# Kernel tuning notes

Measured on AMD Instinct MI355X. Metric: run time of the kernel, lower is better.

Reference implementation:

```python
import jax, jax.numpy as jnp
import numpy as np

H = 128
N0 = 32768
N1 = 32768
N = N0 + N1
E = 524288
R = 4
L = 2
BS = 1024
PER = N // BS


def setup_inputs() -> dict:
    key = jax.random.key(0)
    ks = jax.random.split(key, 20)
    s = 1.0 / np.sqrt(H)
    x0 = jax.random.normal(ks[0], (N0, H), jnp.float32)
    x1 = jax.random.normal(ks[1], (N1, H), jnp.float32)
    W0 = jax.random.normal(ks[2], (H, H), jnp.float32) * s
    W1 = jax.random.normal(ks[3], (H, H), jnp.float32) * s
    conv_root = jax.random.normal(ks[4], (L, H, H), jnp.float32) * s
    conv_rel = jax.random.normal(ks[5], (L, R, H, H), jnp.float32) * s
    attW = jax.random.normal(ks[6], (L, R * R, H, H), jnp.float32) * s
    att_q = jax.random.normal(ks[7], (L, R * R, H), jnp.float32) * s
    att_k = jax.random.normal(ks[8], (L, R * R, H), jnp.float32) * s
    fc_W = jax.random.normal(ks[9], (H, H), jnp.float32) * s
    src = jax.random.randint(ks[10], (E,), 0, N)
    dst = jax.random.randint(ks[11], (E,), 0, N)
    edge_index = jnp.stack([src, dst], 0)
    edge_type = jax.random.randint(ks[12], (E,), 0, R)
    # mask: ones, but zero the first node of ~half the samples (mirrors torch.rand(batch)<0.5)
    drop = jax.random.uniform(ks[13], (BS,)) < 0.5
    row_mask = jnp.where(drop[:, None, None] & (jnp.arange(PER)[None, :, None] == 0), 0.0, 1.0)
    mask = jnp.broadcast_to(row_mask, (BS, PER, H)).reshape(N, H).astype(jnp.float32)
    return {
        "x0": x0, "x1": x1, "W0": W0, "b0": jnp.zeros((H,), jnp.float32),
        "W1": W1, "b1": jnp.zeros((H,), jnp.float32), "mask": mask,
        "conv_root": conv_root, "conv_rel": conv_rel, "conv_b": jnp.zeros((L, H), jnp.float32),
        "attW": attW, "att_q": att_q, "att_k": att_k, "att_b": jnp.zeros((L, H), jnp.float32),
        "bn_g": jnp.ones((L, H), jnp.float32), "bn_b": jnp.zeros((L, H), jnp.float32),
        "fc_W": fc_W, "fc_b": jnp.zeros((H,), jnp.float32),
        "edge_index": edge_index, "edge_type": edge_type, "batch_size": BS,
    }


def reference(x0, x1, W0, b0, W1, b1, mask, conv_root, conv_rel, conv_b,
              attW, att_q, att_k, att_b, bn_g, bn_b, fc_W, fc_b,
              edge_index, edge_type, batch_size):
    n = x0.shape[0] + x1.shape[0]
    r = conv_rel.shape[1]
    # per-node-type linear transforms, then to_homogeneous concat
    x_in = jnp.concatenate([x0 @ W0 + b0, x1 @ W1 + b1], axis=0)  # [N,H]
    src, dst = edge_index[0], edge_index[1]
    seg = dst * r + edge_type  # (target node, relation) segments
    x = x_in
    for l in range(conv_root.shape[0]):
        xm = x * mask
        # ---- RGCNConv: per-relation transform, mean aggregation per relation, root + bias
        xr = jnp.einsum('nh,rho->rno', xm, conv_rel[l])  # [R,N,H]
        m = xr[edge_type, src]  # [E,H]
        s = jax.ops.segment_sum(m, seg, num_segments=n * r)
        cnt = jax.ops.segment_sum(jnp.ones((seg.shape[0],), m.dtype), seg, num_segments=n * r)
        agg = (s / jnp.maximum(cnt, 1.0)[:, None]).reshape(n, r, -1).sum(1)
        x_conv = agg + xm @ conv_root[l] + conv_b[l]
        # ---- RGATConv (heads=1, within-relation softmax, additive self-attention)
        xa = jnp.einsum('nh,rho->rno', xm, attW[l, :r])  # only real edge types used
        sq = jnp.einsum('rnh,rh->rn', xa, att_q[l, :r])
        sk = jnp.einsum('rnh,rh->rn', xa, att_k[l, :r])
        logit = jax.nn.leaky_relu(sq[edge_type, dst] + sk[edge_type, src], 0.2)  # [E]
        mx = jax.ops.segment_max(logit, seg, num_segments=n * r)
        mx = jnp.where(jnp.isfinite(mx), mx, 0.0)
        ex = jnp.exp(logit - mx[seg])
        den = jax.ops.segment_sum(ex, seg, num_segments=n * r)
        alpha = ex / jnp.maximum(den[seg], 1e-16)
        x_att = jax.ops.segment_sum(alpha[:, None] * xa[edge_type, src], dst, num_segments=n) + att_b[l]
        # ---- BatchNorm (training stats) + leaky_relu(0.01)
        h = x_conv + x_att
        mu = h.mean(0)
        var = h.var(0)
        h = (h - mu) / jnp.sqrt(var + 1e-5) * bn_g[l] + bn_b[l]
        x = jax.nn.leaky_relu(h, 0.01)
    out = (x + x_in) @ fc_W + fc_b
    out = out.reshape(batch_size, -1, out.shape[-1])
    return out[:, 0], out[:, 1:, :]
```

## Files before the change

kernel.cpp:

```cpp
#include <hip/hip_runtime.h>

#define Hd 128
#define NTOT 65536
#define RREL 4
#define NRSEG (NTOT*RREL)
#define NEDGE 524288

typedef unsigned short u16;
typedef unsigned int u32;
typedef short bf16x8 __attribute__((ext_vector_type(8)));
typedef float f32x4 __attribute__((ext_vector_type(4)));

__device__ __forceinline__ u16 f2bf(float f) {
  u32 u = __float_as_uint(f);
  return (u16)((u + 0x7fffu + ((u >> 16) & 1u)) >> 16);
}
__device__ __forceinline__ u32 pack2(float lo, float hi) {
  return ((u32)f2bf(hi) << 16) | f2bf(lo);
}

__device__ __forceinline__ int swzb(int row, int o) {
  return (row*256 + o) ^ ((row & 15) << 4);
}

__device__ __forceinline__ void stage_tile(const u16* __restrict__ g, int ld,
                                           u16* lds, int wave, int lane) {
#pragma unroll
  for (int t = 0; t < 2; ++t) {
    int i = wave*2 + t;
    int row = i*16 + (lane >> 2);
    int col16 = (lane & 3) ^ ((lane >> 3) & 3);
    const u16* src = g + (size_t)row*ld + col16*8;
    __builtin_amdgcn_global_load_lds((const __attribute__((address_space(1))) void*)src,
                                     (__attribute__((address_space(3))) void*)(lds + i*512),
                                     16, 0, 0);
  }
}

template<int CMODE>
__global__ __launch_bounds__(256) void mgemm(const u16* __restrict__ A, int lda,
                                             const u16* __restrict__ Bt, int ldb,
                                             const float* __restrict__ bias,
                                             const float* __restrict__ bias2,
                                             float* __restrict__ C, int kTot)
{
  __shared__ u16 As[4096], Bs[4096];
  const int tid = threadIdx.x, wave = tid >> 6, lane = tid & 63;
  const int wm = wave >> 1, wn = wave & 1;
  int bx = blockIdx.x;
  if (CMODE == 3) {
    if (bx >= (int)gridDim.x/2) {
      bx -= gridDim.x/2;
      A += (size_t)32768*lda; Bt += 128*128; bias = bias2; C += (size_t)32768*Hd;
    }
  }
  const int brow = bx * 128;
  const u16* Ab = A + (size_t)brow*lda;
  f32x4 acc[4][4];
#pragma unroll
  for (int i = 0; i < 4; ++i)
#pragma unroll
    for (int j = 0; j < 4; ++j) acc[i][j] = (f32x4){0.f, 0.f, 0.f, 0.f};

  const int ks = (lane >> 4) * 16;
  const int rl = lane & 15;
  for (int k0 = 0; k0 < kTot; k0 += 32) {
    stage_tile(Ab + k0, lda, As, wave, lane);
    stage_tile(Bt + k0, ldb, Bs, wave, lane);
    __syncthreads();
    bf16x8 af[4], bv[4];
    const char* Ac = (const char*)As;
    const char* Bc = (const char*)Bs;
#pragma unroll
    for (int i = 0; i < 4; ++i) {
      int r = wm*64 + i*16 + rl;
      int by = (r*64 + ks) ^ (((r >> 1) & 3) << 4);
      af[i] = *(const bf16x8*)(Ac + by);
    }
#pragma unroll
    for (int j = 0; j < 4; ++j) {
      int r = wn*64 + j*16 + rl;
      int by = (r*64 + ks) ^ (((r >> 1) & 3) << 4);
      bv[j] = *(const bf16x8*)(Bc + by);
    }
#pragma unroll
    for (int i = 0; i < 4; ++i)
#pragma unroll
      for (int j = 0; j < 4; ++j)
        acc[i][j] = __builtin_amdgcn_mfma_f32_16x16x32_bf16(af[i], bv[j], acc[i][j], 0, 0, 0);
    __syncthreads();
  }
  const int cl = lane & 15;
  const int rq = (lane >> 4) * 4;
#pragma unroll
  for (int i = 0; i < 4; ++i) {
#pragma unroll
    for (int q = 0; q < 4; ++q) {
      int row = brow + wm*64 + i*16 + rq + q;
      size_t ob;
      if (CMODE == 2) {
        int b = row >> 6, p = row & 63;
        ob = (p == 0) ? (size_t)b*Hd
                      : (size_t)(1024*Hd) + ((size_t)(b*63 + (p-1)))*Hd;
      } else {
        ob = (size_t)row * Hd;
      }
#pragma unroll
      for (int j = 0; j < 4; ++j) {
        int col = wn*64 + j*16 + cl;
        float v = acc[i][j][q];
        if (bias) v += bias[col];
        C[ob + col] = v;
      }
    }
  }
}

__device__ __forceinline__ void stageB(const u16* __restrict__ gbase, int ld,
                                       u16* lds, int wave, int lane) {
#pragma unroll
  for (int t = 0; t < 4; ++t) {
    int ti = wave*4 + t;
    int row = ti*4 + (lane >> 4);
    int lchunk = (lane & 15) ^ (row & 15);
    const u16* src = gbase + (size_t)row*ld + lchunk*8;
    __builtin_amdgcn_global_load_lds((const __attribute__((address_space(1))) void*)src,
                                     (__attribute__((address_space(3))) void*)(lds + ti*512),
                                     16, 0, 0);
  }
}
__device__ __forceinline__ void stageY64(const u16* __restrict__ gbase, int ld,
                                         u16* lds, int wave, int lane) {
#pragma unroll
  for (int t = 0; t < 2; ++t) {
    int ti = wave*2 + t;
    int row = ti*4 + (lane >> 4);
    int lchunk = (lane & 15) ^ (row & 15);
    const u16* src = gbase + (size_t)row*ld + lchunk*8;
    __builtin_amdgcn_global_load_lds((const __attribute__((address_space(1))) void*)src,
                                     (__attribute__((address_space(3))) void*)(lds + ti*512),
                                     16, 0, 0);
  }
}

__device__ __forceinline__ void mfma64(const u16* Yt, const u16* Bt, f32x4 (&acc)[2][2],
                                       int wm, int wn, int lane) {
  const int rl = lane & 15;
  const int ko = (lane >> 4) * 16;
  const char* Yc_ = (const char*)Yt;
  const char* Bc_ = (const char*)Bt;
#pragma unroll
  for (int ks = 0; ks < 4; ++ks) {
    int o = ks*64 + ko;
    bf16x8 af[2], bv[2];
#pragma unroll
    for (int i = 0; i < 2; ++i)
      af[i] = *(const bf16x8*)(Yc_ + swzb(wm*32 + i*16 + rl, o));
#pragma unroll
    for (int j = 0; j < 2; ++j)
      bv[j] = *(const bf16x8*)(Bc_ + swzb(wn*32 + j*16 + rl, o));
#pragma unroll
    for (int i = 0; i < 2; ++i)
#pragma unroll
      for (int j = 0; j < 2; ++j)
        acc[i][j] = __builtin_amdgcn_mfma_f32_16x16x32_bf16(af[i], bv[j], acc[i][j], 0, 0, 0);
  }
}

__global__ __launch_bounds__(512, 2) void fused_gemm(
    const u16* __restrict__ xmb, const int* __restrict__ src_sorted,
    const float* __restrict__ exs, const int* __restrict__ offsets,
    const u16* __restrict__ Btg, float* __restrict__ hbuf, float* __restrict__ bns)
{
  __shared__ u16 Yt[8192];
  __shared__ u16 Bw[16384];
  const int tid = threadIdx.x, wave = tid >> 6, lane = tid & 63;
  const int wm = wave >> 2, wn = wave & 3;
  const int brow = blockIdx.x * 64;
  f32x4 acc[2][2];
#pragma unroll
  for (int i = 0; i < 2; ++i)
#pragma unroll
    for (int j = 0; j < 2; ++j) acc[i][j] = (f32x4){0.f, 0.f, 0.f, 0.f};

  u32 axp[8];

  for (int r = 0; r < RREL; ++r) {
    __syncthreads();
    stageB(Btg + r*128, 1152, Bw, wave, lane);
#pragma unroll
    for (int g = 0; g < 4; ++g) {
      int ln0 = wave*8 + g*2;
      int e0[2], ct[2];
#pragma unroll
      for (int m = 0; m < 2; ++m) {
        int seg = (brow + ln0 + m)*RREL + r;
        e0[m] = offsets[seg];
        ct[m] = offsets[seg+1] - e0[m];
      }
      int   si[2][4];
      float ew[2][4];
#pragma unroll
      for (int m = 0; m < 2; ++m)
#pragma unroll
        for (int k = 0; k < 4; ++k) {
          si[m][k] = src_sorted[e0[m] + k];
          ew[m][k] = exs[e0[m] + k];
        }
      u32 uu[2][4];
#pragma unroll
      for (int m = 0; m < 2; ++m)
#pragma unroll
        for (int k = 0; k < 4; ++k) {
          int sx = (k < ct[m]) ? si[m][k] : 0;
          uu[m][k] = *(const u32*)(xmb + (size_t)sx*Hd + lane*2);
        }
      float cx[2], cy[2], ax[2], ay[2];
#pragma unroll
      for (int m = 0; m < 2; ++m) { cx[m] = cy[m] = ax[m] = ay[m] = 0.f; }
#pragma unroll
      for (int m = 0; m < 2; ++m) {
#pragma unroll
        for (int k = 0; k < 4; ++k) {
          float pr = (k < ct[m]) ? 1.f : 0.f;
          float al = pr * ew[m][k];
          float vx = __uint_as_float(uu[m][k] << 16);
          float vy = __uint_as_float(uu[m][k] & 0xffff0000u);
          cx[m] = fmaf(pr, vx, cx[m]);
          cy[m] = fmaf(pr, vy, cy[m]);
          ax[m] = fmaf(al, vx, ax[m]);
          ay[m] = fmaf(al, vy, ay[m]);
        }
        for (int e = e0[m] + 4; e < e0[m] + ct[m]; ++e) {
          int s = src_sorted[e];
          float al = exs[e];
          u32 u = *(const u32*)(xmb + (size_t)s*Hd + lane*2);
          float vx = __uint_as_float(u << 16);
          float vy = __uint_as_float(u & 0xffff0000u);
          cx[m] += vx; cy[m] += vy;
          ax[m] = fmaf(al, vx, ax[m]);
          ay[m] = fmaf(al, vy, ay[m]);
        }
      }
#pragma unroll
      for (int m = 0; m < 2; ++m) {
        int ln = ln0 + m;
        float ic = 1.f / (float)max(ct[m], 1);
        *(u32*)((char*)Yt + swzb(ln, lane*4)) = pack2(cx[m]*ic, cy[m]*ic);
        axp[g*2+m] = pack2(ax[m], ay[m]);
      }
    }
    __syncthreads();
    mfma64(Yt, Bw, acc, wm, wn, lane);
    __syncthreads();
    stageB(Btg + (4+r)*128, 1152, Bw, wave, lane);
#pragma unroll
    for (int g = 0; g < 4; ++g)
#pragma unroll
      for (int m = 0; m < 2; ++m) {
        int ln = wave*8 + g*2 + m;
        *(u32*)((char*)Yt + swzb(ln, lane*4)) = axp[g*2+m];
      }
    __syncthreads();
    mfma64(Yt, Bw, acc, wm, wn, lane);
  }
  __syncthreads();
  stageY64(xmb + (size_t)brow*Hd, Hd, Yt, wave, lane);
  stageB(Btg + 8*128, 1152, Bw, wave, lane);
  __syncthreads();
  mfma64(Yt, Bw, acc, wm, wn, lane);

  const int cl = lane & 15, rq = (lane >> 4) * 4;
#pragma unroll
  for (int j = 0; j < 2; ++j) {
    float s = 0.f, s2 = 0.f;
#pragma unroll
    for (int i = 0; i < 2; ++i) {
#pragma unroll
      for (int q = 0; q < 4; ++q) {
        float v = acc[i][j][q];
        int row = brow + wm*32 + i*16 + rq + q;
        hbuf[(size_t)row*Hd + wn*32 + j*16 + cl] = v;
        s += v; s2 = fmaf(v, v, s2);
      }
    }
    s  += __shfl_xor(s, 16);  s  += __shfl_xor(s, 32);
    s2 += __shfl_xor(s2, 16); s2 += __shfl_xor(s2, 32);
    if (lane < 16) {
      int col = wn*32 + j*16 + cl;
      unsafeAtomicAdd(&bns[col], s);
      unsafeAtomicAdd(&bns[128 + col], s2);
    }
  }
}

__global__ void wtrans(const float* __restrict__ B, u16* __restrict__ Bt,
                       int K, int ldb, int koff) {
  int idx = blockIdx.x*256 + threadIdx.x;
  if (idx >= K*128) return;
  int k = idx >> 7, o = idx & 127;
  Bt[(size_t)o*ldb + koff + k] = f2bf(B[idx]);
}

__global__ void fill_i32(int* p, int v, int n) {
  int i = blockIdx.x*blockDim.x + threadIdx.x;
  if (i < n) p[i] = v;
}
__global__ void rowmask_k(const float* __restrict__ mask, float* __restrict__ rm) {
  int n = blockIdx.x*blockDim.x + threadIdx.x;
  if (n < NTOT) rm[n] = mask[(size_t)n*Hd];
}
__global__ void edge_count(const int* __restrict__ dst, const int* __restrict__ et, int* __restrict__ cnt) {
  int e = blockIdx.x*blockDim.x + threadIdx.x;
  if (e < NEDGE) atomicAdd(&cnt[dst[e]*RREL + et[e]], 1);
}
__global__ void cvt_bf16_2(const float* __restrict__ s0, const float* __restrict__ s1,
                           u16* __restrict__ dst) {
  int i = blockIdx.x*256 + threadIdx.x;
  const int half = 32768*Hd/4;
  const float* s = (i < half) ? s0 : s1;
  int ii = (i < half) ? i : i - half;
  float4 v = *reinterpret_cast<const float4*>(s + (size_t)ii*4);
  *reinterpret_cast<uint2*>(dst + (size_t)i*4) = make_uint2(pack2(v.x, v.y), pack2(v.z, v.w));
}
__global__ void mkxmb(const float* __restrict__ x, const float* __restrict__ rm,
                      u16* __restrict__ xmb) {
  int i = blockIdx.x*256 + threadIdx.x;
  float s = rm[i >> 5];
  float4 v = *reinterpret_cast<const float4*>(x + (size_t)i*4);
  *reinterpret_cast<uint2*>(xmb + (size_t)i*4) =
      make_uint2(pack2(v.x*s, v.y*s), pack2(v.z*s, v.w*s));
}

__global__ void scan1_k(const int* __restrict__ cnt, int* __restrict__ partial, int* __restrict__ bsum) {
  __shared__ int sh[256];
  int t = threadIdx.x;
  int i = blockIdx.x*256 + t;
  int v = cnt[i];
  sh[t] = v; __syncthreads();
  for (int off = 1; off < 256; off <<= 1) {
    int u = (t >= off) ? sh[t-off] : 0;
    __syncthreads();
    sh[t] += u;
    __syncthreads();
  }
  partial[i] = sh[t] - v;
  if (t == 255) bsum[blockIdx.x] = sh[255];
}
__global__ void scan2_k(int* __restrict__ bsum) {
  __shared__ int sh[256];
  int t = threadIdx.x;
  int v0 = bsum[t*4+0], v1 = bsum[t*4+1], v2 = bsum[t*4+2], v3 = bsum[t*4+3];
  int tot = v0+v1+v2+v3;
  sh[t] = tot; __syncthreads();
  for (int off = 1; off < 256; off <<= 1) {
    int u = (t >= off) ? sh[t-off] : 0;
    __syncthreads();
    sh[t] += u;
    __syncthreads();
  }
  int base = sh[t] - tot;
  bsum[t*4+0] = base;
  bsum[t*4+1] = base + v0;
  bsum[t*4+2] = base + v0+v1;
  bsum[t*4+3] = base + v0+v1+v2;
}
__global__ void scan3_k(const int* __restrict__ partial, const int* __restrict__ bsum, int* __restrict__ offsets) {
  int i = blockIdx.x*256 + threadIdx.x;
  offsets[i] = partial[i] + bsum[i >> 8];
  if (i == 0) offsets[NRSEG] = NEDGE;
}
__global__ void csr_fill(const int* __restrict__ src, const int* __restrict__ dst,
                         const int* __restrict__ et, const int* __restrict__ offsets,
                         int* __restrict__ fillctr, int* __restrict__ src_sorted) {
  int e = blockIdx.x*blockDim.x + threadIdx.x;
  if (e >= NEDGE) return;
  int seg = dst[e]*RREL + et[e];
  int pos = offsets[seg] + atomicAdd(&fillctr[seg], 1);
  src_sorted[pos] = src[e];
}

__global__ void qkvec_k(const float* __restrict__ attW, const float* __restrict__ att_q,
                        const float* __restrict__ att_k,
                        float* __restrict__ qvec, float* __restrict__ kvec,
                        float* __restrict__ bns) {
  int t = threadIdx.x;
  if (t < 256) bns[t] = 0.f;
  int r = t >> 7, h = t & 127;
  const float* wrow = attW + ((size_t)r*Hd + h)*Hd;
  const float* qv = att_q + (size_t)r*Hd;
  const float* kv = att_k + (size_t)r*Hd;
  float sq_ = 0.f, sk_ = 0.f;
  for (int o = 0; o < Hd; ++o) { float w = wrow[o]; sq_ = fmaf(w, qv[o], sq_); sk_ = fmaf(w, kv[o], sk_); }
  qvec[r*Hd + h] = sq_;
  kvec[r*Hd + h] = sk_;
}

__global__ void sqk_k(const u16* __restrict__ xmb, const float* __restrict__ qvec,
                      const float* __restrict__ kvec, float* __restrict__ sq, float* __restrict__ sk) {
  int w = blockIdx.x*4 + (threadIdx.x >> 6);
  if (w >= NTOT) return;
  int lane = threadIdx.x & 63;
  u32 u = *reinterpret_cast<const u32*>(xmb + (size_t)w*Hd + lane*2);
  float vx = __uint_as_float(u << 16);
  float vy = __uint_as_float(u & 0xffff0000u);
  float pq[RREL], pk[RREL];
#pragma unroll
  for (int r = 0; r < RREL; ++r) {
    float2 q = *reinterpret_cast<const float2*>(qvec + r*Hd + lane*2);
    float2 k = *reinterpret_cast<const float2*>(kvec + r*Hd + lane*2);
    pq[r] = vx*q.x + vy*q.y;
    pk[r] = vx*k.x + vy*k.y;
  }
#pragma unroll
  for (int off = 32; off > 0; off >>= 1) {
#pragma unroll
    for (int r = 0; r < RREL; ++r) {
      pq[r] += __shfl_xor(pq[r], off);
      pk[r] += __shfl_xor(pk[r], off);
    }
  }
  if (lane == 0) {
#pragma unroll
    for (int r = 0; r < RREL; ++r) {
      sq[(size_t)r*NTOT + w] = pq[r];
      sk[(size_t)r*NTOT + w] = pk[r];
    }
  }
}

__global__ void seg_alpha(const int* __restrict__ src_sorted, const int* __restrict__ offsets,
                          const float* __restrict__ sq, const float* __restrict__ sk,
                          float* __restrict__ exs) {
  int seg = blockIdx.x*256 + threadIdx.x;
  if (seg >= NRSEG) return;
  int e0 = offsets[seg], e1 = offsets[seg+1];
  if (e0 == e1) return;
  int nd = seg >> 2, r = seg & 3;
  float sqv = sq[(size_t)r*NTOT + nd];
  float sum = 0.f;
  for (int e = e0; e < e1; ++e) {
    float lg = sqv + sk[(size_t)r*NTOT + src_sorted[e]];
    lg = lg >= 0.f ? lg : 0.2f*lg;
    float ex = __expf(lg);
    exs[e] = ex;
    sum += ex;
  }
  float inv = 1.f / fmaxf(sum, 1e-16f);
  for (int e = e0; e < e1; ++e) exs[e] *= inv;
}

__global__ void bn_final(const float* __restrict__ bns, const float* __restrict__ g,
                         const float* __restrict__ b, float* __restrict__ scale,
                         float* __restrict__ shift) {
  int c = threadIdx.x;
  float mu = bns[c] * (1.f/NTOT);
  float var = bns[128 + c] * (1.f/NTOT) - mu*mu;
  float sc = g[c] / sqrtf(var + 1e-5f);
  scale[c] = sc;
  shift[c] = b[c] - mu*sc;
}

template<int LAST>
__global__ void bn_apply(const float* __restrict__ h, const float* __restrict__ scale,
                         const float* __restrict__ shift, const float* __restrict__ rm,
                         const float* __restrict__ x_in, u16* __restrict__ xmb) {
  int i = blockIdx.x*256 + threadIdx.x;
  size_t i4 = (size_t)i*4;
  int c = (int)(i4 & 127);
  float4 v = *reinterpret_cast<const float4*>(h + i4);
  float4 sc = *reinterpret_cast<const float4*>(scale + c);
  float4 sh = *reinterpret_cast<const float4*>(shift + c);
  v.x = fmaf(v.x, sc.x, sh.x); v.y = fmaf(v.y, sc.y, sh.y);
  v.z = fmaf(v.z, sc.z, sh.z); v.w = fmaf(v.w, sc.w, sh.w);
  v.x = v.x >= 0.f ? v.x : 0.01f*v.x;
  v.y = v.y >= 0.f ? v.y : 0.01f*v.y;
  v.z = v.z >= 0.f ? v.z : 0.01f*v.z;
  v.w = v.w >= 0.f ? v.w : 0.01f*v.w;
  float4 xb;
  if (LAST) {
    float4 rsd = *reinterpret_cast<const float4*>(x_in + i4);
    xb.x = v.x + rsd.x; xb.y = v.y + rsd.y; xb.z = v.z + rsd.z; xb.w = v.w + rsd.w;
  } else {
    float s = rm[i >> 5];
    xb.x = v.x*s; xb.y = v.y*s; xb.z = v.z*s; xb.w = v.w*s;
  }
  *reinterpret_cast<uint2*>(xmb + i4) = make_uint2(pack2(xb.x, xb.y), pack2(xb.z, xb.w));
}

extern "C" void kernel_launch(void* const* d_in, const int* in_sizes, int n_in,
                              void* d_out, int out_size, void* d_ws, size_t ws_size,
                              hipStream_t stream) {
  const float* x0       = (const float*)d_in[0];
  const float* x1       = (const float*)d_in[1];
  const float* W0       = (const float*)d_in[2];
  const float* b0       = (const float*)d_in[3];
  const float* W1       = (const float*)d_in[4];
  const float* b1       = (const float*)d_in[5];
  const float* mask     = (const float*)d_in[6];
  const float* conv_root= (const float*)d_in[7];
  const float* conv_rel = (const float*)d_in[8];
  const float* attW     = (const float*)d_in[10];
  const float* att_q    = (const float*)d_in[11];
  const float* att_k    = (const float*)d_in[12];
  const float* bn_g     = (const float*)d_in[14];
  const float* bn_b     = (const float*)d_in[15];
  const float* fc_W     = (const float*)d_in[16];
  const float* fc_b     = (const float*)d_in[17];
  const int* edge_index = (const int*)d_in[18];
  const int* edge_type  = (const int*)d_in[19];
  const int* src = edge_index;
  const int* dst = edge_index + NEDGE;
  (void)in_sizes; (void)n_in; (void)out_size; (void)ws_size;

  char* ws = (char*)d_ws;
  size_t off = 0;
  auto alloc = [&](size_t bytes) { void* p = ws + off; off = (off + bytes + 255) & ~(size_t)255; return p; };
  float* x_in  = (float*)alloc((size_t)NTOT*Hd*4);
  float* hbuf  = (float*)alloc((size_t)NTOT*Hd*4);
  u16*   xmb   = (u16*)  alloc((size_t)NTOT*Hd*2);
  float* sq    = (float*)alloc((size_t)RREL*NTOT*4);
  float* sk    = (float*)alloc((size_t)RREL*NTOT*4);
  float* exs   = (float*)alloc((size_t)(NEDGE+16)*4);
  float* rm    = (float*)alloc((size_t)NTOT*4);
  int* cnt        = (int*)alloc((size_t)NRSEG*4);
  int* fillctr    = (int*)alloc((size_t)NRSEG*4);
  int* partial    = (int*)alloc((size_t)NRSEG*4);
  int* offsets    = (int*)alloc((size_t)(NRSEG+4)*4);
  int* bsum       = (int*)alloc(4096);
  int* src_sorted = (int*)alloc((size_t)(NEDGE+16)*4);
  float* qvec   = (float*)alloc(512*4);
  float* kvec   = (float*)alloc(512*4);
  float* bns    = (float*)alloc(1024);
  float* bnscale= (float*)alloc(512);
  float* bnshift= (float*)alloc(512);
  u16* Btw  = (u16*)alloc((size_t)2*128*128*2);
  u16* Btg0 = (u16*)alloc((size_t)128*1152*2);
  u16* Btg1 = (u16*)alloc((size_t)128*1152*2);
  u16* BtgL[2] = {Btg0, Btg1};

  rowmask_k<<<NTOT/256, 256, 0, stream>>>(mask, rm);
  fill_i32<<<NRSEG/256, 256, 0, stream>>>(cnt, 0, NRSEG);
  edge_count<<<NEDGE/256, 256, 0, stream>>>(dst, edge_type, cnt);
  scan1_k<<<NRSEG/256, 256, 0, stream>>>(cnt, partial, bsum);
  scan2_k<<<1, 256, 0, stream>>>(bsum);
  scan3_k<<<NRSEG/256, 256, 0, stream>>>(partial, bsum, offsets);
  fill_i32<<<NRSEG/256, 256, 0, stream>>>(fillctr, 0, NRSEG);
  csr_fill<<<NEDGE/256, 256, 0, stream>>>(src, dst, edge_type, offsets, fillctr, src_sorted);

  for (int l = 0; l < 2; ++l) {
    wtrans<<<(512*128)/256, 256, 0, stream>>>(conv_rel + (size_t)l*RREL*Hd*Hd, BtgL[l], 512, 1152, 0);
    wtrans<<<(512*128)/256, 256, 0, stream>>>(attW + (size_t)l*16*Hd*Hd, BtgL[l], 512, 1152, 512);
    wtrans<<<(128*128)/256, 256, 0, stream>>>(conv_root + (size_t)l*Hd*Hd, BtgL[l], 128, 1152, 1024);
  }

  cvt_bf16_2<<<(NTOT*Hd/4)/256, 256, 0, stream>>>(x0, x1, xmb);
  wtrans<<<(128*128)/256, 256, 0, stream>>>(W0, Btw, 128, 128, 0);
  wtrans<<<(128*128)/256, 256, 0, stream>>>(W1, Btw + 128*128, 128, 128, 0);
  mgemm<3><<<512, 256, 0, stream>>>(xmb, Hd, Btw, 128, b0, b1, x_in, 128);
  mkxmb<<<(NTOT*Hd/4)/256, 256, 0, stream>>>(x_in, rm, xmb);

  for (int l = 0; l < 2; ++l) {
    const float* attW_l = attW + (size_t)l*16*Hd*Hd;
    qkvec_k<<<1, 512, 0, stream>>>(attW_l, att_q + (size_t)l*16*Hd, att_k + (size_t)l*16*Hd,
                                   qvec, kvec, bns);
    sqk_k<<<NTOT/4, 256, 0, stream>>>(xmb, qvec, kvec, sq, sk);
    seg_alpha<<<NRSEG/256, 256, 0, stream>>>(src_sorted, offsets, sq, sk, exs);
    fused_gemm<<<NTOT/64, 512, 0, stream>>>(xmb, src_sorted, exs, offsets,
                                            BtgL[l], hbuf, bns);
    bn_final<<<1, 128, 0, stream>>>(bns, bn_g + (size_t)l*Hd, bn_b + (size_t)l*Hd, bnscale, bnshift);
    if (l == 0)
      bn_apply<0><<<(NTOT*Hd/4)/256, 256, 0, stream>>>(hbuf, bnscale, bnshift, rm, x_in, xmb);
    else
      bn_apply<1><<<(NTOT*Hd/4)/256, 256, 0, stream>>>(hbuf, bnscale, bnshift, rm, x_in, xmb);
  }

  wtrans<<<(128*128)/256, 256, 0, stream>>>(fc_W, Btw, 128, 128, 0);
  mgemm<2><<<512, 256, 0, stream>>>(xmb, Hd, Btw, 128, fc_b, nullptr, (float*)d_out, 128);
}
```

Measured before the change: 482.3 us.

## Restructure RGCN layer kernels with relation-major CSR and LDS atomic aggregation

Switches the segment layout to relation-major and packs source and destination into one 32-bit meta word per edge. The fused GEMM now handles 32 rows per block and spreads edge aggregation across waves using float atomics in LDS, instead of per-node loops in registers. Separately, weight transposes are merged into one launch, q/k vectors for both layers are precomputed, and the BN apply is fused with the attention-score computation. This cuts launch count, tail imbalance on uneven degrees and a full pass over xmb, at the cost of LDS atomic contention and a 16-bit packing limit on node ids.

```diff
diff --git a/kernel.cpp b/kernel.cpp
--- a/kernel.cpp
+++ b/kernel.cpp
@@ -129,21 +129,17 @@
                                      16, 0, 0);
   }
 }
-__device__ __forceinline__ void stageY64(const u16* __restrict__ gbase, int ld,
+__device__ __forceinline__ void stageY32(const u16* __restrict__ gbase, int ld,
                                          u16* lds, int wave, int lane) {
-#pragma unroll
-  for (int t = 0; t < 2; ++t) {
-    int ti = wave*2 + t;
-    int row = ti*4 + (lane >> 4);
-    int lchunk = (lane & 15) ^ (row & 15);
-    const u16* src = gbase + (size_t)row*ld + lchunk*8;
-    __builtin_amdgcn_global_load_lds((const __attribute__((address_space(1))) void*)src,
-                                     (__attribute__((address_space(3))) void*)(lds + ti*512),
-                                     16, 0, 0);
-  }
-}
-
-__device__ __forceinline__ void mfma64(const u16* Yt, const u16* Bt, f32x4 (&acc)[2][2],
+  int row = wave*4 + (lane >> 4);
+  int lchunk = (lane & 15) ^ (row & 15);
+  const u16* src = gbase + (size_t)row*ld + lchunk*8;
+  __builtin_amdgcn_global_load_lds((const __attribute__((address_space(1))) void*)src,
+                                   (__attribute__((address_space(3))) void*)(lds + wave*512),
+                                   16, 0, 0);
+}
+
+__device__ __forceinline__ void mfma32(const u16* Yt, const u16* Bt, f32x4 (&acc)[2],
                                        int wm, int wn, int lane) {
   const int rl = lane & 15;
   const int ko = (lane >> 4) * 16;
@@ -152,137 +148,116 @@
 #pragma unroll
   for (int ks = 0; ks < 4; ++ks) {
     int o = ks*64 + ko;
-    bf16x8 af[2], bv[2];
-#pragma unroll
-    for (int i = 0; i < 2; ++i)
-      af[i] = *(const bf16x8*)(Yc_ + swzb(wm*32 + i*16 + rl, o));
-#pragma unroll
-    for (int j = 0; j < 2; ++j)
-      bv[j] = *(const bf16x8*)(Bc_ + swzb(wn*32 + j*16 + rl, o));
-#pragma unroll
-    for (int i = 0; i < 2; ++i)
-#pragma unroll
-      for (int j = 0; j < 2; ++j)
-        acc[i][j] = __builtin_amdgcn_mfma_f32_16x16x32_bf16(af[i], bv[j], acc[i][j], 0, 0, 0);
+    bf16x8 af = *(const bf16x8*)(Yc_ + swzb(wm*16 + rl, o));
+    bf16x8 b0 = *(const bf16x8*)(Bc_ + swzb(wn*32 + rl, o));
+    bf16x8 b1 = *(const bf16x8*)(Bc_ + swzb(wn*32 + 16 + rl, o));
+    acc[0] = __builtin_amdgcn_mfma_f32_16x16x32_bf16(af, b0, acc[0], 0, 0, 0);
+    acc[1] = __builtin_amdgcn_mfma_f32_16x16x32_bf16(af, b1, acc[1], 0, 0, 0);
   }
 }
 
 __global__ __launch_bounds__(512, 2) void fused_gemm(
-    const u16* __restrict__ xmb, const int* __restrict__ src_sorted,
+    const u16* __restrict__ xmb, const u32* __restrict__ meta,
     const float* __restrict__ exs, const int* __restrict__ offsets,
     const u16* __restrict__ Btg, float* __restrict__ hbuf, float* __restrict__ bns)
 {
-  __shared__ u16 Yt[8192];
-  __shared__ u16 Bw[16384];
+  __shared__ float Ycf[4096];
+  __shared__ float Yaf[4096];
+  __shared__ u16  Ybf[4096];
+  __shared__ u16  Bw[16384];
   const int tid = threadIdx.x, wave = tid >> 6, lane = tid & 63;
   const int wm = wave >> 2, wn = wave & 3;
-  const int brow = blockIdx.x * 64;
-  f32x4 acc[2][2];
-#pragma unroll
-  for (int i = 0; i < 2; ++i)
-#pragma unroll
-    for (int j = 0; j < 2; ++j) acc[i][j] = (f32x4){0.f, 0.f, 0.f, 0.f};
-
-  u32 axp[8];
+  const int brow = blockIdx.x * 32;
+  f32x4 acc[2];
+  acc[0] = (f32x4){0.f,0.f,0.f,0.f};
+  acc[1] = (f32x4){0.f,0.f,0.f,0.f};
+
+  {
+    float4 z = {0.f,0.f,0.f,0.f};
+#pragma unroll
+    for (int t = 0; t < 2; ++t) {
+      *(float4*)(Ycf + tid*4 + t*2048) = z;
+      *(float4*)(Yaf + tid*4 + t*2048) = z;
+    }
+  }
+  const int prow = tid >> 4;
+  const int pc2  = (tid & 15) * 8;
+  const int pX   = (prow & 7) << 2;
 
   for (int r = 0; r < RREL; ++r) {
+    const int segBase = (r << 16) + brow;
     __syncthreads();
     stageB(Btg + r*128, 1152, Bw, wave, lane);
-#pragma unroll
-    for (int g = 0; g < 4; ++g) {
-      int ln0 = wave*8 + g*2;
-      int e0[2], ct[2];
-#pragma unroll
-      for (int m = 0; m < 2; ++m) {
-        int seg = (brow + ln0 + m)*RREL + r;
-        e0[m] = offsets[seg];
-        ct[m] = offsets[seg+1] - e0[m];
+    float ic;
+    {
+      int a = offsets[segBase + prow], b = offsets[segBase + prow + 1];
+      ic = 1.f / (float)max(b - a, 1);
+    }
+    {
+      int eB = offsets[segBase], eE = offsets[segBase + 32];
+      for (int e = eB + wave; e < eE; e += 8) {
+        u32 md = meta[e];
+        float al = exs[e];
+        int s  = md & 0xffff;
+        int ln = (int)(md >> 16) - brow;
+        u32 u = *(const u32*)(xmb + ((size_t)s << 7) + lane*2);
+        float vx = __uint_as_float(u << 16);
+        float vy = __uint_as_float(u & 0xffff0000u);
+        int fi = ((ln << 7) + lane*2) ^ ((ln & 7) << 2);
+        unsafeAtomicAdd(&Ycf[fi],     vx);
+        unsafeAtomicAdd(&Ycf[fi + 1], vy);
+        unsafeAtomicAdd(&Yaf[fi],     al*vx);
+        unsafeAtomicAdd(&Yaf[fi + 1], al*vy);
       }
-      int   si[2][4];
-      float ew[2][4];
-#pragma unroll
-      for (int m = 0; m < 2; ++m)
-#pragma unroll
-        for (int k = 0; k < 4; ++k) {
-          si[m][k] = src_sorted[e0[m] + k];
-          ew[m][k] = exs[e0[m] + k];
-        }
-      u32 uu[2][4];
-#pragma unroll
-      for (int m = 0; m < 2; ++m)
-#pragma unroll
-        for (int k = 0; k < 4; ++k) {
-          int sx = (k < ct[m]) ? si[m][k] : 0;
-          uu[m][k] = *(const u32*)(xmb + (size_t)sx*Hd + lane*2);
-        }
-      float cx[2], cy[2], ax[2], ay[2];
-#pragma unroll
-      for (int m = 0; m < 2; ++m) { cx[m] = cy[m] = ax[m] = ay[m] = 0.f; }
-#pragma unroll
-      for (int m = 0; m < 2; ++m) {
-#pragma unroll
-        for (int k = 0; k < 4; ++k) {
-          float pr = (k < ct[m]) ? 1.f : 0.f;
-          float al = pr * ew[m][k];
-          float vx = __uint_as_float(uu[m][k] << 16);
-          float vy = __uint_as_float(uu[m][k] & 0xffff0000u);
-          cx[m] = fmaf(pr, vx, cx[m]);
-          cy[m] = fmaf(pr, vy, cy[m]);
-          ax[m] = fmaf(al, vx, ax[m]);
-          ay[m] = fmaf(al, vy, ay[m]);
-        }
-        for (int e = e0[m] + 4; e < e0[m] + ct[m]; ++e) {
-          int s = src_sorted[e];
-          float al = exs[e];
-          u32 u = *(const u32*)(xmb + (size_t)s*Hd + lane*2);
-          float vx = __uint_as_float(u << 16);
-          float vy = __uint_as_float(u & 0xffff0000u);
-          cx[m] += vx; cy[m] += vy;
-          ax[m] = fmaf(al, vx, ax[m]);
-          ay[m] = fmaf(al, vy, ay[m]);
-        }
-      }
-#pragma unroll
-      for (int m = 0; m < 2; ++m) {
-        int ln = ln0 + m;
-        float ic = 1.f / (float)max(ct[m], 1);
-        *(u32*)((char*)Yt + swzb(ln, lane*4)) = pack2(cx[m]*ic, cy[m]*ic);
-        axp[g*2+m] = pack2(ax[m], ay[m]);
-      }
-    }
-    __syncthreads();
-    mfma64(Yt, Bw, acc, wm, wn, lane);
+    }
+    __syncthreads();
+    {
+      int base = prow*128 + pc2;
+      int i0 = base ^ pX, i1 = (base + 4) ^ pX;
+      float4 v0 = *(float4*)(Ycf + i0);
+      float4 v1 = *(float4*)(Ycf + i1);
+      *(float4*)(Ycf + i0) = (float4){0.f,0.f,0.f,0.f};
+      *(float4*)(Ycf + i1) = (float4){0.f,0.f,0.f,0.f};
+      uint4 o;
+      o.x = pack2(v0.x*ic, v0.y*ic); o.y = pack2(v0.z*ic, v0.w*ic);
+      o.z = pack2(v1.x*ic, v1.y*ic); o.w = pack2(v1.z*ic, v1.w*ic);
+      *(uint4*)((char*)Ybf + swzb(prow, pc2*2)) = o;
+    }
+    __syncthreads();
+    mfma32(Ybf, Bw, acc, wm, wn, lane);
     __syncthreads();
     stageB(Btg + (4+r)*128, 1152, Bw, wave, lane);
-#pragma unroll
-    for (int g = 0; g < 4; ++g)
-#pragma unroll
-      for (int m = 0; m < 2; ++m) {
-        int ln = wave*8 + g*2 + m;
-        *(u32*)((char*)Yt + swzb(ln, lane*4)) = axp[g*2+m];
-      }
-    __syncthreads();
-    mfma64(Yt, Bw, acc, wm, wn, lane);
+    {
+      int base = prow*128 + pc2;
+      int i0 = base ^ pX, i1 = (base + 4) ^ pX;
+      float4 v0 = *(float4*)(Yaf + i0);
+      float4 v1 = *(float4*)(Yaf + i1);
+      *(float4*)(Yaf + i0) = (float4){0.f,0.f,0.f,0.f};
+      *(float4*)(Yaf + i1) = (float4){0.f,0.f,0.f,0.f};
+      uint4 o;
+      o.x = pack2(v0.x, v0.y); o.y = pack2(v0.z, v0.w);
+      o.z = pack2(v1.x, v1.y); o.w = pack2(v1.z, v1.w);
+      *(uint4*)((char*)Ybf + swzb(prow, pc2*2)) = o;
+    }
+    __syncthreads();
+    mfma32(Ybf, Bw, acc, wm, wn, lane);
   }
   __syncthreads();
-  stageY64(xmb + (size_t)brow*Hd, Hd, Yt, wave, lane);
+  stageY32(xmb + ((size_t)brow << 7), Hd, Ybf, wave, lane);
   stageB(Btg + 8*128, 1152, Bw, wave, lane);
   __syncthreads();
-  mfma64(Yt, Bw, acc, wm, wn, lane);
+  mfma32(Ybf, Bw, acc, wm, wn, lane);
 
   const int cl = lane & 15, rq = (lane >> 4) * 4;
 #pragma unroll
   for (int j = 0; j < 2; ++j) {
     float s = 0.f, s2 = 0.f;
 #pragma unroll
-    for (int i = 0; i < 2; ++i) {
-#pragma unroll
-      for (int q = 0; q < 4; ++q) {
-        float v = acc[i][j][q];
-        int row = brow + wm*32 + i*16 + rq + q;
-        hbuf[(size_t)row*Hd + wn*32 + j*16 + cl] = v;
-        s += v; s2 = fmaf(v, v, s2);
-      }
+    for (int q = 0; q < 4; ++q) {
+      float v = acc[j][q];
+      int row = brow + wm*16 + rq + q;
+      hbuf[(size_t)row*Hd + wn*32 + j*16 + cl] = v;
+      s += v; s2 = fmaf(v, v, s2);
     }
     s  += __shfl_xor(s, 16);  s  += __shfl_xor(s, 32);
     s2 += __shfl_xor(s2, 16); s2 += __shfl_xor(s2, 32);
@@ -294,12 +269,27 @@
   }
 }
 
-__global__ void wtrans(const float* __restrict__ B, u16* __restrict__ Bt,
-                       int K, int ldb, int koff) {
+__global__ void wtrans_all(const float* __restrict__ conv_rel, const float* __restrict__ attW,
+                           const float* __restrict__ conv_root, const float* __restrict__ W0,
+                           const float* __restrict__ W1, const float* __restrict__ fcW,
+                           u16* __restrict__ Btg0, u16* __restrict__ Btg1, u16* __restrict__ Btw) {
   int idx = blockIdx.x*256 + threadIdx.x;
-  if (idx >= K*128) return;
-  int k = idx >> 7, o = idx & 127;
-  Bt[(size_t)o*ldb + koff + k] = f2bf(B[idx]);
+  if (idx < 294912) {
+    int l = idx / 147456;
+    int rem = idx - l*147456;
+    u16* Btg = l ? Btg1 : Btg0;
+    float v; int o, kk;
+    if (rem < 65536)       { o = rem & 127; kk = rem >> 7;               v = conv_rel[(size_t)l*65536 + rem]; }
+    else if (rem < 131072) { int r2 = rem - 65536; o = r2 & 127; kk = 512 + (r2 >> 7); v = attW[(size_t)l*262144 + r2]; }
+    else                   { int r3 = rem - 131072; o = r3 & 127; kk = 1024 + (r3 >> 7); v = conv_root[(size_t)l*16384 + r3]; }
+    Btg[(size_t)o*1152 + kk] = f2bf(v);
+  } else {
+    int rem = idx - 294912;
+    int w = rem >> 14, r3 = rem & 16383;
+    int k = r3 >> 7, o = r3 & 127;
+    const float* sp = (w == 0) ? W0 : (w == 1 ? W1 : fcW);
+    Btw[w*16384 + o*128 + k] = f2bf(sp[r3]);
+  }
 }
 
 __global__ void fill_i32(int* p, int v, int n) {
@@ -312,7 +302,7 @@
 }
 __global__ void edge_count(const int* __restrict__ dst, const int* __restrict__ et, int* __restrict__ cnt) {
   int e = blockIdx.x*blockDim.x + threadIdx.x;
-  if (e < NEDGE) atomicAdd(&cnt[dst[e]*RREL + et[e]], 1);
+  if (e < NEDGE) atomicAdd(&cnt[(et[e] << 16) + dst[e]], 1);
 }
 __global__ void cvt_bf16_2(const float* __restrict__ s0, const float* __restrict__ s1,
                            u16* __restrict__ dst) {
@@ -323,14 +313,6 @@
   float4 v = *reinterpret_cast<const float4*>(s + (size_t)ii*4);
   *reinterpret_cast<uint2*>(dst + (size_t)i*4) = make_uint2(pack2(v.x, v.y), pack2(v.z, v.w));
 }
-__global__ void mkxmb(const float* __restrict__ x, const float* __restrict__ rm,
-                      u16* __restrict__ xmb) {
-  int i = blockIdx.x*256 + threadIdx.x;
-  float s = rm[i >> 5];
-  float4 v = *reinterpret_cast<const float4*>(x + (size_t)i*4);
-  *reinterpret_cast<uint2*>(xmb + (size_t)i*4) =
-      make_uint2(pack2(v.x*s, v.y*s), pack2(v.z*s, v.w*s));
-}
 
 __global__ void scan1_k(const int* __restrict__ cnt, int* __restrict__ partial, int* __restrict__ bsum) {
   __shared__ int sh[256];
@@ -372,75 +354,96 @@
 }
 __global__ void csr_fill(const int* __restrict__ src, const int* __restrict__ dst,
                          const int* __restrict__ et, const int* __restrict__ offsets,
-                         int* __restrict__ fillctr, int* __restrict__ src_sorted) {
+                         int* __restrict__ fillctr, u32* __restrict__ meta) {
   int e = blockIdx.x*blockDim.x + threadIdx.x;
   if (e >= NEDGE) return;
-  int seg = dst[e]*RREL + et[e];
+  int d = dst[e];
+  int seg = (et[e] << 16) + d;
   int pos = offsets[seg] + atomicAdd(&fillctr[seg], 1);
-  src_sorted[pos] = src[e];
-}
-
-__global__ void qkvec_k(const float* __restrict__ attW, const float* __restrict__ att_q,
-                        const float* __restrict__ att_k,
-                        float* __restrict__ qvec, float* __restrict__ kvec,
-                        float* __restrict__ bns) {
-  int t = threadIdx.x;
-  if (t < 256) bns[t] = 0.f;
-  int r = t >> 7, h = t & 127;
-  const float* wrow = attW + ((size_t)r*Hd + h)*Hd;
-  const float* qv = att_q + (size_t)r*Hd;
-  const float* kv = att_k + (size_t)r*Hd;
+  meta[pos] = (u32)src[e] | ((u32)d << 16);
+}
+
+__global__ void qkvec_all(const float* __restrict__ attW, const float* __restrict__ att_q,
+                          const float* __restrict__ att_k,
+                          float* __restrict__ qvecL, float* __restrict__ kvecL) {
+  int l = blockIdx.x;
+  const float* aW = attW + (size_t)l*16*Hd*Hd;
+  const float* aq = att_q + (size_t)l*16*Hd;
+  const float* ak = att_k + (size_t)l*16*Hd;
+  int r = threadIdx.x >> 7, h = threadIdx.x & 127;
+  const float* wrow = aW + ((size_t)r*Hd + h)*Hd;
+  const float* qv = aq + (size_t)r*Hd;
+  const float* kv = ak + (size_t)r*Hd;
   float sq_ = 0.f, sk_ = 0.f;
   for (int o = 0; o < Hd; ++o) { float w = wrow[o]; sq_ = fmaf(w, qv[o], sq_); sk_ = fmaf(w, kv[o], sk_); }
-  qvec[r*Hd + h] = sq_;
-  kvec[r*Hd + h] = sk_;
-}
-
-__global__ void sqk_k(const u16* __restrict__ xmb, const float* __restrict__ qvec,
-                      const float* __restrict__ kvec, float* __restrict__ sq, float* __restrict__ sk) {
-  int w = blockIdx.x*4 + (threadIdx.x >> 6);
-  if (w >= NTOT) return;
+  qvecL[l*512 + r*Hd + h] = sq_;
+  kvecL[l*512 + r*Hd + h] = sk_;
+}
+
+template<int MODE>
+__global__ __launch_bounds__(256) void xform_sqk(
+    const float* __restrict__ hin, const float* __restrict__ scale,
+    const float* __restrict__ shift, const float* __restrict__ rm,
+    const float* __restrict__ x_in, const float* __restrict__ qvec,
+    const float* __restrict__ kvec, u16* __restrict__ xmb,
+    float* __restrict__ sq, float* __restrict__ sk)
+{
+  int n = blockIdx.x*4 + (threadIdx.x >> 6);
   int lane = threadIdx.x & 63;
-  u32 u = *reinterpret_cast<const u32*>(xmb + (size_t)w*Hd + lane*2);
-  float vx = __uint_as_float(u << 16);
-  float vy = __uint_as_float(u & 0xffff0000u);
-  float pq[RREL], pk[RREL];
-#pragma unroll
-  for (int r = 0; r < RREL; ++r) {
-    float2 q = *reinterpret_cast<const float2*>(qvec + r*Hd + lane*2);
-    float2 k = *reinterpret_cast<const float2*>(kvec + r*Hd + lane*2);
-    pq[r] = vx*q.x + vy*q.y;
-    pk[r] = vx*k.x + vy*k.y;
-  }
-#pragma unroll
-  for (int off = 32; off > 0; off >>= 1) {
+  float2 v = *(const float2*)(hin + (size_t)n*Hd + lane*2);
+  if (MODE != 0) {
+    float2 sc = *(const float2*)(scale + lane*2);
+    float2 sh = *(const float2*)(shift + lane*2);
+    v.x = fmaf(v.x, sc.x, sh.x); v.y = fmaf(v.y, sc.y, sh.y);
+    v.x = v.x >= 0.f ? v.x : 0.01f*v.x;
+    v.y = v.y >= 0.f ? v.y : 0.01f*v.y;
+  }
+  float2 xb;
+  if (MODE == 2) {
+    float2 rs = *(const float2*)(x_in + (size_t)n*Hd + lane*2);
+    xb.x = v.x + rs.x; xb.y = v.y + rs.y;
+  } else {
+    float s = rm[n];
+    xb.x = v.x*s; xb.y = v.y*s;
+  }
+  *(u32*)(xmb + (size_t)n*Hd + lane*2) = pack2(xb.x, xb.y);
+  if (MODE != 2) {
+    float pq[RREL], pk[RREL];
 #pragma unroll
     for (int r = 0; r < RREL; ++r) {
-      pq[r] += __shfl_xor(pq[r], off);
-      pk[r] += __shfl_xor(pk[r], off);
-    }
-  }
-  if (lane == 0) {
-#pragma unroll
-    for (int r = 0; r < RREL; ++r) {
-      sq[(size_t)r*NTOT + w] = pq[r];
-      sk[(size_t)r*NTOT + w] = pk[r];
-    }
-  }
-}
-
-__global__ void seg_alpha(const int* __restrict__ src_sorted, const int* __restrict__ offsets,
+      float2 q = *(const float2*)(qvec + r*Hd + lane*2);
+      float2 k = *(const float2*)(kvec + r*Hd + lane*2);
+      pq[r] = xb.x*q.x + xb.y*q.y;
+      pk[r] = xb.x*k.x + xb.y*k.y;
+    }
+#pragma unroll
+    for (int off = 32; off > 0; off >>= 1)
+#pragma unroll
+      for (int r = 0; r < RREL; ++r) {
+        pq[r] += __shfl_xor(pq[r], off);
+        pk[r] += __shfl_xor(pk[r], off);
+      }
+    if (lane == 0)
+#pragma unroll
+      for (int r = 0; r < RREL; ++r) {
+        sq[(size_t)r*NTOT + n] = pq[r];
+        sk[(size_t)r*NTOT + n] = pk[r];
+      }
+  }
+}
+
+__global__ void seg_alpha(const u32* __restrict__ meta, const int* __restrict__ offsets,
                           const float* __restrict__ sq, const float* __restrict__ sk,
-                          float* __restrict__ exs) {
+                          float* __restrict__ exs, float* __restrict__ bns) {
   int seg = blockIdx.x*256 + threadIdx.x;
-  if (seg >= NRSEG) return;
+  if (blockIdx.x == 0 && threadIdx.x < 256) bns[threadIdx.x] = 0.f;
   int e0 = offsets[seg], e1 = offsets[seg+1];
   if (e0 == e1) return;
-  int nd = seg >> 2, r = seg & 3;
-  float sqv = sq[(size_t)r*NTOT + nd];
+  const float* skr = sk + (seg & 0xFFFF0000u);
+  float sqv = sq[seg];
   float sum = 0.f;
   for (int e = e0; e < e1; ++e) {
-    float lg = sqv + sk[(size_t)r*NTOT + src_sorted[e]];
+    float lg = sqv + skr[meta[e] & 0xffff];
     lg = lg >= 0.f ? lg : 0.2f*lg;
     float ex = __expf(lg);
     exs[e] = ex;
@@ -459,33 +462,6 @@
   float sc = g[c] / sqrtf(var + 1e-5f);
   scale[c] = sc;
   shift[c] = b[c] - mu*sc;
-}
-
-template<int LAST>
-__global__ void bn_apply(const float* __restrict__ h, const float* __restrict__ scale,
-                         const float* __restrict__ shift, const float* __restrict__ rm,
-                         const float* __restrict__ x_in, u16* __restrict__ xmb) {
-  int i = blockIdx.x*256 + threadIdx.x;
-  size_t i4 = (size_t)i*4;
-  int c = (int)(i4 & 127);
-  float4 v = *reinterpret_cast<const float4*>(h + i4);
-  float4 sc = *reinterpret_cast<const float4*>(scale + c);
-  float4 sh = *reinterpret_cast<const float4*>(shift + c);
-  v.x = fmaf(v.x, sc.x, sh.x); v.y = fmaf(v.y, sc.y, sh.y);
-  v.z = fmaf(v.z, sc.z, sh.z); v.w = fmaf(v.w, sc.w, sh.w);
-  v.x = v.x >= 0.f ? v.x : 0.01f*v.x;
-  v.y = v.y >= 0.f ? v.y : 0.01f*v.y;
-  v.z = v.z >= 0.f ? v.z : 0.01f*v.z;
-  v.w = v.w >= 0.f ? v.w : 0.01f*v.w;
-  float4 xb;
-  if (LAST) {
-    float4 rsd = *reinterpret_cast<const float4*>(x_in + i4);
-    xb.x = v.x + rsd.x; xb.y = v.y + rsd.y; xb.z = v.z + rsd.z; xb.w = v.w + rsd.w;
-  } else {
-    float s = rm[i >> 5];
-    xb.x = v.x*s; xb.y = v.y*s; xb.z = v.z*s; xb.w = v.w*s;
-  }
-  *reinterpret_cast<uint2*>(xmb + i4) = make_uint2(pack2(xb.x, xb.y), pack2(xb.z, xb.w));
 }
 
 extern "C" void kernel_launch(void* const* d_in, const int* in_sizes, int n_in,
@@ -521,20 +497,20 @@
   u16*   xmb   = (u16*)  alloc((size_t)NTOT*Hd*2);
   float* sq    = (float*)alloc((size_t)RREL*NTOT*4);
   float* sk    = (float*)alloc((size_t)RREL*NTOT*4);
-  float* exs   = (float*)alloc((size_t)(NEDGE+16)*4);
+  float* exs   = (float*)alloc((size_t)NEDGE*4);
   float* rm    = (float*)alloc((size_t)NTOT*4);
-  int* cnt        = (int*)alloc((size_t)NRSEG*4);
-  int* fillctr    = (int*)alloc((size_t)NRSEG*4);
-  int* partial    = (int*)alloc((size_t)NRSEG*4);
-  int* offsets    = (int*)alloc((size_t)(NRSEG+4)*4);
-  int* bsum       = (int*)alloc(4096);
-  int* src_sorted = (int*)alloc((size_t)(NEDGE+16)*4);
-  float* qvec   = (float*)alloc(512*4);
-  float* kvec   = (float*)alloc(512*4);
+  int* cnt     = (int*)alloc((size_t)NRSEG*4);
+  int* fillctr = (int*)alloc((size_t)NRSEG*4);
+  int* partial = (int*)alloc((size_t)NRSEG*4);
+  int* offsets = (int*)alloc((size_t)(NRSEG+4)*4);
+  int* bsum    = (int*)alloc(4096);
+  u32* meta    = (u32*)alloc((size_t)NEDGE*4);
+  float* qvecL = (float*)alloc(2*512*4);
+  float* kvecL = (float*)alloc(2*512*4);
   float* bns    = (float*)alloc(1024);
   float* bnscale= (float*)alloc(512);
   float* bnshift= (float*)alloc(512);
-  u16* Btw  = (u16*)alloc((size_t)2*128*128*2);
+  u16* Btw  = (u16*)alloc((size_t)3*128*128*2);
   u16* Btg0 = (u16*)alloc((size_t)128*1152*2);
   u16* Btg1 = (u16*)alloc((size_t)128*1152*2);
   u16* BtgL[2] = {Btg0, Btg1};
@@ -546,35 +522,29 @@
   scan2_k<<<1, 256, 0, stream>>>(bsum);
   scan3_k<<<NRSEG/256, 256, 0, stream>>>(partial, bsum, offsets);
   fill_i32<<<NRSEG/256, 256, 0, stream>>>(fillctr, 0, NRSEG);
-  csr_fill<<<NEDGE/256, 256, 0, stream>>>(src, dst, edge_type, offsets, fillctr, src_sorted);
+  csr_fill<<<NEDGE/256, 256, 0, stream>>>(src, dst, edge_type, offsets, fillctr, meta);
+
+  wtrans_all<<<1344, 256, 0, stream>>>(conv_rel, attW, conv_root, W0, W1, fc_W,
+                                       Btg0, Btg1, Btw);
+  qkvec_all<<<2, 512, 0, stream>>>(attW, att_q, att_k, qvecL, kvecL);
+
+  cvt_bf16_2<<<(NTOT*Hd/4)/256, 256, 0, stream>>>(x0, x1, xmb);
+  mgemm<3><<<512, 256, 0, stream>>>(xmb, Hd, Btw, 128, b0, b1, x_in, 128);
+  xform_sqk<0><<<NTOT/4, 256, 0, stream>>>(x_in, nullptr, nullptr, rm, nullptr,
+                                           qvecL, kvecL, xmb, sq, sk);
 
   for (int l = 0; l < 2; ++l) {
-    wtrans<<<(512*128)/256, 256, 0, stream>>>(conv_rel + (size_t)l*RREL*Hd*Hd, BtgL[l], 512, 1152, 0);
-    wtrans<<<(512*128)/256, 256, 0, stream>>>(attW + (size_t)l*16*Hd*Hd, BtgL[l], 512, 1152, 512);
-    wtrans<<<(128*128)/256, 256, 0, stream>>>(conv_root + (size_t)l*Hd*Hd, BtgL[l], 128, 1152, 1024);
-  }
-
-  cvt_bf16_2<<<(NTOT*Hd/4)/256, 256, 0, stream>>>(x0, x1, xmb);
-  wtrans<<<(128*128)/256, 256, 0, stream>>>(W0, Btw, 128, 128, 0);
-  wtrans<<<(128*128)/256, 256, 0, stream>>>(W1, Btw + 128*128, 128, 128, 0);
-  mgemm<3><<<512, 256, 0, stream>>>(xmb, Hd, Btw, 128, b0, b1, x_in, 128);
-  mkxmb<<<(NTOT*Hd/4)/256, 256, 0, stream>>>(x_in, rm, xmb);
-
-  for (int l = 0; l < 2; ++l) {
-    const float* attW_l = attW + (size_t)l*16*Hd*Hd;
-    qkvec_k<<<1, 512, 0, stream>>>(attW_l, att_q + (size_t)l*16*Hd, att_k + (size_t)l*16*Hd,
-                                   qvec, kvec, bns);
-    sqk_k<<<NTOT/4, 256, 0, stream>>>(xmb, qvec, kvec, sq, sk);
-    seg_alpha<<<NRSEG/256, 256, 0, stream>>>(src_sorted, offsets, sq, sk, exs);
-    fused_gemm<<<NTOT/64, 512, 0, stream>>>(xmb, src_sorted, exs, offsets,
-                                            BtgL[l], hbuf, bns);
+    seg_alpha<<<NRSEG/256, 256, 0, stream>>>(meta, offsets, sq, sk, exs, bns);
+    fused_gemm<<<NTOT/32, 512, 0, stream>>>(xmb, meta, exs, offsets, BtgL[l], hbuf, bns);
     bn_final<<<1, 128, 0, stream>>>(bns, bn_g + (size_t)l*Hd, bn_b + (size_t)l*Hd, bnscale, bnshift);
     if (l == 0)
-      bn_apply<0><<<(NTOT*Hd/4)/256, 256, 0, stream>>>(hbuf, bnscale, bnshift, rm, x_in, xmb);
+      xform_sqk<1><<<NTOT/4, 256, 0, stream>>>(hbuf, bnscale, bnshift, rm, nullptr,
+                                               qvecL + 512, kvecL + 512, xmb, sq, sk);
     else
-      bn_apply<1><<<(NTOT*Hd/4)/256, 256, 0, stream>>>(hbuf, bnscale, bnshift, rm, x_in, xmb);
-  }
-
-  wtrans<<<(128*128)/256, 256, 0, stream>>>(fc_W, Btw, 128, 128, 0);
-  mgemm<2><<<512, 256, 0, stream>>>(xmb, Hd, Btw, 128, fc_b, nullptr, (float*)d_out, 128);
-}
+      xform_sqk<2><<<NTOT/4, 256, 0, stream>>>(hbuf, bnscale, bnshift, nullptr, x_in,
+                                               nullptr, nullptr, xmb, sq, sk);
+  }
+
+  mgemm<2><<<512, 256, 0, stream>>>(xmb, Hd, Btw + 2*16384, 128, fc_b, nullptr,
+                                    (float*)d_out, 128);
+}
```

After: 1.734 ms. 260% more time.
